# Optimization experiments

Hardware: AMD Instinct MI355X
Metric: run time of the kernel (lower is better)

The kernel has to match this reference:

```python
import jax, jax.numpy as jnp
import numpy as np

K = 5            # neighborhood kernel size
PAD = 2
CENTER = (K * K) // 2   # index 12: the pixel itself
TEMP = 0.1       # InfoNCE temperature
EPS = 1e-8
NUM_CLASSES = 2


def _patches_f(x):
    """x: [B,H,W,C] float -> [B,H,W,K*K,C] zero-padded 5x5 neighborhoods."""
    B, H, W, C = x.shape
    xp = jnp.pad(x, ((0, 0), (PAD, PAD), (PAD, PAD), (0, 0)))
    return jnp.stack([xp[:, i:i + H, j:j + W, :]
                      for i in range(K) for j in range(K)], axis=3)


def _patches_i(x):
    """x: [B,H,W] int -> [B,H,W,K*K] zero-padded 5x5 neighborhoods."""
    B, H, W = x.shape
    xp = jnp.pad(x, ((0, 0), (PAD, PAD), (PAD, PAD)))
    return jnp.stack([xp[:, i:i + H, j:j + W]
                      for i in range(K) for j in range(K)], axis=3)


def setup_inputs() -> dict:
    key = jax.random.key(0)
    k1, k2, k3, k4 = jax.random.split(key, 4)
    B, C, H, W = 2, 256, 96, 96
    return {
        "er_input": jax.random.normal(k1, (B, C, H, W), dtype=jnp.float32),
        "seg_logit": jax.random.normal(k2, (B, NUM_CLASSES, H, W), dtype=jnp.float32),
        "seg_label": jax.random.randint(k3, (B, H, W), 0, NUM_CLASSES, dtype=jnp.int32),
        "gt_boundary_seg": jax.random.randint(k4, (B, H, W), 0, 2, dtype=jnp.int32),
    }


def reference(er_input, seg_logit, seg_label, gt_boundary_seg):
    # er_input: [B,C,H,W]; seg_logit: [B,nc,H,W]; labels: [B,H,W]
    feat = er_input.transpose(0, 2, 3, 1)          # [B,H,W,C]
    pred = jnp.argmax(seg_logit, axis=1)           # [B,H,W]
    gt_b = jnp.where(gt_boundary_seg == 255, 0, gt_boundary_seg)
    edge = gt_b.astype(bool)                       # boundary mask [B,H,W]

    neigh_feat = _patches_f(feat)                  # [B,H,W,25,C]
    neigh_label = _patches_i(seg_label)            # [B,H,W,25]
    neigh_pred = _patches_i(pred)                  # [B,H,W,25]

    def correct(c):
        # one_hot(label)*one_hot(pred) at class c, per neighbor
        return ((neigh_label == c) & (neigh_pred == c)).astype(feat.dtype)

    a_norm_neigh = jnp.linalg.norm(neigh_feat, axis=-1)   # [B,H,W,25]

    total = jnp.asarray(0.0, dtype=feat.dtype)
    shown = list(range(NUM_CLASSES))               # shown_class (both assumed present)
    n_cls = len(shown)
    for i in range(n_cls):
        c = shown[i]
        c_pre = shown[(i - 1) % n_cls]
        c_post = shown[(i + 1) % n_cls]

        now_mask = (seg_label == c)                # [B,H,W]
        neigh_is_c = (neigh_label == c).astype(feat.dtype)
        # same-class neighbor count, center excluded (kernel has 0 at center)
        count = neigh_is_c.sum(-1) - neigh_is_c[..., CENTER]
        pix_mask = ((count >= 1) & edge & now_mask).astype(feat.dtype)  # [B,H,W]

        w_now = correct(c)                         # [B,H,W,25]
        w_neg = correct(c_pre) + correct(c_post)   # pre_class + post_class weights

        # anchor = center feature * correct indicator (taken before zeroing center)
        anchor = neigh_feat[..., CENTER, :] * w_now[..., CENTER, None]  # [B,H,W,C]
        # positive = mean over 25 neighbors of (feat * correct), center zeroed
        positive = (jnp.einsum('bhwkc,bhwk->bhwc', neigh_feat, w_now) - anchor) / (K * K)

        a_norm = jnp.linalg.norm(anchor, axis=-1)  # [B,H,W]
        p_norm = jnp.linalg.norm(positive, axis=-1)
        pos_cos = (anchor * positive).sum(-1) / (a_norm * p_norm + EPS)   # [B,H,W]

        # negatives: per-offset features weighted by (pre+post) correctness
        dots = jnp.einsum('bhwc,bhwkc->bhwk', anchor, neigh_feat)         # [B,H,W,25]
        neg_cos = (dots * w_neg) / (a_norm[..., None] * a_norm_neigh * w_neg + EPS)

        logits = jnp.concatenate([pos_cos[..., None], neg_cos], axis=-1) / TEMP
        loss_pix = -jax.nn.log_softmax(logits, axis=-1)[..., 0]          # [B,H,W]

        total = total + (loss_pix * pix_mask).sum() / jnp.maximum(pix_mask.sum(), 1.0)
    return total
```

## Files before the change

### kernel.cpp

```cpp
#include <hip/hip_runtime.h>
#include <math.h>

#define Hc 96
#define Wc 96
#define Bc 2
#define Cc 256
#define HWc (Hc * Wc)
#define NKc 25
#define NPIX (Bc * HWc)
#define NSLOT 32

#define OFF_ACC 0
#define OFF_CNT 256
#define OFF_MIS 264
#define OFF_HC 272
#define OFF_DONE 276
#define HDR_FLOATS 80
#define OFF_NRM2 320
#define OFF_META (OFF_NRM2 + 2 * NPIX * 4)
#define OFF_WL (OFF_META + NPIX)
#define OFF_FT (OFF_WL + NPIX * 16)

__device__ __forceinline__ float wave_reduce_sum(float v) {
#pragma unroll
  for (int off = 32; off > 0; off >>= 1) v += __shfl_xor(v, off);
  return v;
}

#define NOFF(k) (((k) / 5 - 2) * Wc + ((k) % 5 - 2))

__device__ __forceinline__ unsigned f2bf_pack(float lo, float hi) {
  unsigned a = __float_as_uint(lo), b = __float_as_uint(hi);
  a = (a + 0x7FFFu + ((a >> 16) & 1u)) >> 16;
  b = (b + 0x7FFFu + ((b >> 16) & 1u)) >> 16;
  return a | (b << 16);
}
__device__ __forceinline__ float bf2f(unsigned short u) {
  return __uint_as_float(((unsigned)u) << 16);
}

__global__ __launch_bounds__(256) void transpose_kernel(
    const float* __restrict__ in, const float* __restrict__ seg_logit,
    const int* __restrict__ seg_label, unsigned* __restrict__ outb,
    float* __restrict__ nrm2h, unsigned char* __restrict__ meta,
    float* __restrict__ hdr) {
  __shared__ float tile[64][33];
  __shared__ float part[8][32];
  const int bx = blockIdx.x;
  const int b = blockIdx.y;
  const int half = blockIdx.z;
  const int tx = threadIdx.x;
  const int ty = threadIdx.y;
  const float* src = in + (size_t)b * Cc * HWc;
  const int p0 = bx * 32;

  if (bx == 0 && b == 0 && half == 0) {
    const int t = ty * 32 + tx;
    if (t < HDR_FLOATS) hdr[t] = 0.f;
  }

  float psum = 0.f;
  for (int s = 0; s < 2; ++s) {
    const int c0 = half * 128 + s * 64;
#pragma unroll
    for (int i = 0; i < 8; i++)
      tile[ty + i * 8][tx] = src[(size_t)(c0 + ty + i * 8) * HWc + p0 + tx];
    __syncthreads();
#pragma unroll
    for (int i = 0; i < 4; i++) {
      const int px = ty + i * 8;
      const unsigned pk = f2bf_pack(tile[2 * tx][px], tile[2 * tx + 1][px]);
      outb[(size_t)(b * HWc + p0 + px) * (Cc / 2) + (c0 / 2) + tx] = pk;
    }
#pragma unroll
    for (int j = 0; j < 8; j++) {
      const float v = tile[ty * 8 + j][tx];
      psum += v * v;
    }
    __syncthreads();
  }
  part[ty][tx] = psum;
  __syncthreads();
  if (ty == 0) {
    float t = 0.f;
#pragma unroll
    for (int j = 0; j < 8; j++) t += part[j][tx];
    const int hw = p0 + tx;
    const int gi = b * HWc + hw;
    nrm2h[half * NPIX + gi] = t;
    if (half == 0) {
      const float l0 = seg_logit[(size_t)(b * 2 + 0) * HWc + hw];
      const float l1 = seg_logit[(size_t)(b * 2 + 1) * HWc + hw];
      const int pr = (l1 > l0) ? 1 : 0;
      meta[gi] = (unsigned char)((seg_label[gi] & 1) | (pr << 1));
    }
  }
}

__global__ __launch_bounds__(256) void classify_kernel(
    const unsigned char* __restrict__ meta, const int* __restrict__ gtb,
    const float* __restrict__ nrm2h, float* __restrict__ cnt,
    float* __restrict__ mis, unsigned int* __restrict__ heavyCount,
    uint4* __restrict__ worklist) {
  __shared__ unsigned int s_cnt[4];
  if (threadIdx.x < 4) s_cnt[threadIdx.x] = 0;
  __syncthreads();
  const int tid = blockIdx.x * 256 + threadIdx.x;
  bool heavy = false;
  int c = 0;
  unsigned mNow = 0, mNeg = 0;
  float a_norm = 0.f;
  {
    const int hw = tid % HWc;
    const int h = hw / Wc, w = hw % Wc;
    int g = gtb[tid];
    if (g == 255) g = 0;
    if (g) {
      const int m0 = meta[tid];
      c = m0 & 1;
      const int pc = (m0 >> 1) & 1;
      const int oc = 1 - c;
      int count = 0;
#pragma unroll
      for (int k = 0; k < NKc; k++) {
        const int di = k / 5 - 2, dj = k % 5 - 2;
        const int hh = h + di, ww = w + dj;
        const bool inb = (hh >= 0) && (hh < Hc) && (ww >= 0) && (ww < Wc);
        const int mv = inb ? (int)meta[tid + di * Wc + dj] : 0;
        const int lb = mv & 1, pr = (mv >> 1) & 1;
        count += (lb == c);
        if (inb) {
          if (lb == c && pr == c) mNow |= 1u << k;
          if (lb == oc && pr == oc) mNeg |= 1u << k;
        }
      }
      count -= 1;
      if (count >= 1) {
        atomicAdd(&s_cnt[c], 1u);
        if (pc == c) {
          heavy = true;
          a_norm = sqrtf(nrm2h[tid] + nrm2h[NPIX + tid]);
        } else {
          atomicAdd(&s_cnt[2 + c], 1u);
        }
      }
    }
  }
  const unsigned long long m = __ballot(heavy);
  const int lane = threadIdx.x & 63;
  if (m) {
    unsigned int base = 0;
    if (lane == 0) base = atomicAdd(heavyCount, (unsigned)__popcll(m));
    base = __shfl(base, 0);
    if (heavy) {
      const unsigned idx = base + (unsigned)__popcll(m & ((1ull << lane) - 1ull));
      worklist[idx] = make_uint4((unsigned)tid | ((unsigned)c << 16), mNow, mNeg,
                                 __float_as_uint(a_norm));
    }
  }
  __syncthreads();
  if (threadIdx.x < 2) {
    if (s_cnt[threadIdx.x]) atomicAdd(&cnt[threadIdx.x], (float)s_cnt[threadIdx.x]);
    if (s_cnt[2 + threadIdx.x]) atomicAdd(&mis[threadIdx.x], (float)s_cnt[2 + threadIdx.x]);
  }
}

__global__ __launch_bounds__(256, 2) void heavy_kernel(
    const ushort4* __restrict__ ftb, const float* __restrict__ nrm2h,
    const unsigned int* __restrict__ heavyCount,
    const uint4* __restrict__ worklist, float* __restrict__ accum,
    unsigned int* __restrict__ doneCnt, const float* __restrict__ cnt,
    const float* __restrict__ mis, float* __restrict__ out) {
  __shared__ float s_loss[2];
  __shared__ unsigned s_last;
  if (threadIdx.x < 2) s_loss[threadIdx.x] = 0.f;
  __syncthreads();
  const int lane = threadIdx.x & 63;
  const int wv = threadIdx.x >> 6;
  const unsigned nH = *heavyCount;
  const unsigned nw = gridDim.x * 4;
  float lacc0 = 0.f, lacc1 = 0.f;
  for (unsigned i = blockIdx.x * 4 + wv; i < nH; i += nw) {
    const uint4 e = worklist[i];
    const int wid = e.x & 0xffff;
    const int c = (e.x >> 16) & 1;
    const unsigned mNow = e.y, mNeg = e.z;
    const unsigned mAny = mNow | mNeg;
    const float a_norm = __uint_as_float(e.w);

    const int dlt = (lane / 5 - 2) * Wc + (lane % 5 - 2);
    const int nbn = (lane < NKc && ((mNeg >> lane) & 1u)) ? wid + dlt : wid;
    const float nk2a = nrm2h[nbn];
    const float nk2b = nrm2h[NPIX + nbn];
    const ushort4 a4 = ftb[(size_t)wid * 64 + lane];
    ushort4 f4[NKc];
#pragma unroll
    for (int k = 0; k < NKc; k++) {
      const int off = ((mAny >> k) & 1u) ? wid + NOFF(k) : wid;
      f4[k] = ftb[(size_t)off * 64 + lane];
    }
    asm volatile("" ::: "memory");

    const float ax = bf2f(a4.x), ay = bf2f(a4.y), az = bf2f(a4.z), aw = bf2f(a4.w);
    const float nkv = sqrtf(nk2a + nk2b);

    float4 pos = make_float4(0.f, 0.f, 0.f, 0.f);
#pragma unroll
    for (int k = 0; k < NKc; k++) {
      const float wN = (float)((mNow >> k) & 1u);
      pos.x = fmaf(bf2f(f4[k].x), wN, pos.x);
      pos.y = fmaf(bf2f(f4[k].y), wN, pos.y);
      pos.z = fmaf(bf2f(f4[k].z), wN, pos.z);
      pos.w = fmaf(bf2f(f4[k].w), wN, pos.w);
    }
    float4 pv;
    pv.x = (pos.x - ax) * (1.0f / 25.0f);
    pv.y = (pos.y - ay) * (1.0f / 25.0f);
    pv.z = (pos.z - az) * (1.0f / 25.0f);
    pv.w = (pos.w - aw) * (1.0f / 25.0f);
    const float p2 = wave_reduce_sum(pv.x * pv.x + pv.y * pv.y + pv.z * pv.z + pv.w * pv.w);
    const float ad = wave_reduce_sum(ax * pv.x + ay * pv.y + az * pv.z + aw * pv.w);
    const float x0 = (ad / (a_norm * sqrtf(p2) + 1e-8f)) * 10.0f;

    float mx = fmaxf(x0, 0.f);
    float ssum = __expf(x0 - mx) + (float)(NKc - __popc(mNeg)) * __expf(-mx);
#pragma unroll
    for (int k = 0; k < NKc; k++) {
      if ((mNeg >> k) & 1u) {
        const float d = wave_reduce_sum(ax * bf2f(f4[k].x) + ay * bf2f(f4[k].y) +
                                        az * bf2f(f4[k].z) + aw * bf2f(f4[k].w));
        const float nk = __shfl(nkv, k);
        const float x = ((d * 2.0f) / (a_norm * nk * 2.0f + 1e-8f)) * 10.0f;
        if (x > mx) {
          ssum = ssum * __expf(mx - x) + 1.0f;
          mx = x;
        } else {
          ssum += __expf(x - mx);
        }
      }
    }
    const float loss = mx + __logf(ssum) - x0;
    if (lane == 0) {
      if (c == 0) lacc0 += loss; else lacc1 += loss;
    }
  }
  if (lane == 0) {
    if (lacc0 != 0.f) atomicAdd(&s_loss[0], lacc0);
    if (lacc1 != 0.f) atomicAdd(&s_loss[1], lacc1);
  }
  __syncthreads();
  if (threadIdx.x < 2) {
    const float v = s_loss[threadIdx.x];
    if (v != 0.f) atomicAdd(&accum[(blockIdx.x & (NSLOT - 1)) * 2 + threadIdx.x], v);
  }
  __syncthreads();
  if (threadIdx.x == 0)
    s_last = (atomicAdd(doneCnt, 1u) == (unsigned)(gridDim.x - 1)) ? 1u : 0u;
  __syncthreads();
  if (s_last && threadIdx.x < NSLOT * 2) {
    const float v = atomicAdd(&accum[threadIdx.x], 0.0f);
    float v0 = (threadIdx.x & 1) ? 0.f : v;
    float v1 = (threadIdx.x & 1) ? v : 0.f;
    v0 = wave_reduce_sum(v0);
    v1 = wave_reduce_sum(v1);
    if (threadIdx.x == 0) {
      const float LOG26 = logf(26.0f);
      out[0] = (v0 + LOG26 * mis[0]) / fmaxf(cnt[0], 1.0f) +
               (v1 + LOG26 * mis[1]) / fmaxf(cnt[1], 1.0f);
    }
  }
}

extern "C" void kernel_launch(void* const* d_in, const int* in_sizes, int n_in,
                              void* d_out, int out_size, void* d_ws, size_t ws_size,
                              hipStream_t stream) {
  const float* er = (const float*)d_in[0];
  const float* seg_logit = (const float*)d_in[1];
  const int* seg_label = (const int*)d_in[2];
  const int* gtb = (const int*)d_in[3];
  float* out = (float*)d_out;

  char* ws = (char*)d_ws;
  float* hdr = (float*)ws;
  float* accum = (float*)(ws + OFF_ACC);
  float* cnt = (float*)(ws + OFF_CNT);
  float* mis = (float*)(ws + OFF_MIS);
  unsigned int* heavyCount = (unsigned int*)(ws + OFF_HC);
  unsigned int* doneCnt = (unsigned int*)(ws + OFF_DONE);
  float* nrm2h = (float*)(ws + OFF_NRM2);
  unsigned char* meta = (unsigned char*)(ws + OFF_META);
  uint4* worklist = (uint4*)(ws + OFF_WL);
  unsigned* featTb = (unsigned*)(ws + OFF_FT);

  dim3 tb(32, 8, 1);
  dim3 tg(HWc / 32, Bc, 2);
  transpose_kernel<<<tg, tb, 0, stream>>>(er, seg_logit, seg_label, featTb,
                                          nrm2h, meta, hdr);

  classify_kernel<<<NPIX / 256, 256, 0, stream>>>(meta, gtb, nrm2h, cnt, mis,
                                                  heavyCount, worklist);

  heavy_kernel<<<1152, 256, 0, stream>>>((const ushort4*)featTb, nrm2h,
                                         heavyCount, worklist, accum, doneCnt,
                                         cnt, mis, out);
}
```

Measured before the change: 45.53 us.

## Fuse pixel classification into transpose kernel and use dense per-pixel worklist

```diff
diff --git a/kernel.cpp b/kernel.cpp
--- a/kernel.cpp
+++ b/kernel.cpp
@@ -9,17 +9,14 @@
 #define NKc 25
 #define NPIX (Bc * HWc)
 #define NSLOT 32
+#define NBLK 576
 
 #define OFF_ACC 0
-#define OFF_CNT 256
-#define OFF_MIS 264
-#define OFF_HC 272
-#define OFF_DONE 276
-#define HDR_FLOATS 80
-#define OFF_NRM2 320
-#define OFF_META (OFF_NRM2 + 2 * NPIX * 4)
-#define OFF_WL (OFF_META + NPIX)
-#define OFF_FT (OFF_WL + NPIX * 16)
+#define OFF_DONE 256
+#define OFF_CNTB 512
+#define OFF_NRM2 4096
+#define OFF_WL 151552
+#define OFF_FT 446464
 
 __device__ __forceinline__ float wave_reduce_sum(float v) {
 #pragma unroll
@@ -39,25 +36,25 @@
   return __uint_as_float(((unsigned)u) << 16);
 }
 
-__global__ __launch_bounds__(256) void transpose_kernel(
+__global__ __launch_bounds__(256) void transclass_kernel(
     const float* __restrict__ in, const float* __restrict__ seg_logit,
-    const int* __restrict__ seg_label, unsigned* __restrict__ outb,
-    float* __restrict__ nrm2h, unsigned char* __restrict__ meta,
+    const int* __restrict__ seg_label, const int* __restrict__ gtb,
+    unsigned* __restrict__ outb, float* __restrict__ nrm2h,
+    uint4* __restrict__ wl, unsigned* __restrict__ cntBlk,
     float* __restrict__ hdr) {
   __shared__ float tile[64][33];
   __shared__ float part[8][32];
+  __shared__ unsigned s_ccnt[4];
   const int bx = blockIdx.x;
   const int b = blockIdx.y;
   const int half = blockIdx.z;
   const int tx = threadIdx.x;
   const int ty = threadIdx.y;
+  const int flat = ty * 32 + tx;
   const float* src = in + (size_t)b * Cc * HWc;
   const int p0 = bx * 32;
 
-  if (bx == 0 && b == 0 && half == 0) {
-    const int t = ty * 32 + tx;
-    if (t < HDR_FLOATS) hdr[t] = 0.f;
-  }
+  if (bx == 0 && b == 0 && half == 0 && flat < 80) hdr[flat] = 0.f;
 
   float psum = 0.f;
   for (int s = 0; s < 2; ++s) {
@@ -85,109 +82,77 @@
     float t = 0.f;
 #pragma unroll
     for (int j = 0; j < 8; j++) t += part[j][tx];
-    const int hw = p0 + tx;
-    const int gi = b * HWc + hw;
-    nrm2h[half * NPIX + gi] = t;
-    if (half == 0) {
-      const float l0 = seg_logit[(size_t)(b * 2 + 0) * HWc + hw];
-      const float l1 = seg_logit[(size_t)(b * 2 + 1) * HWc + hw];
-      const int pr = (l1 > l0) ? 1 : 0;
-      meta[gi] = (unsigned char)((seg_label[gi] & 1) | (pr << 1));
-    }
-  }
-}
-
-__global__ __launch_bounds__(256) void classify_kernel(
-    const unsigned char* __restrict__ meta, const int* __restrict__ gtb,
-    const float* __restrict__ nrm2h, float* __restrict__ cnt,
-    float* __restrict__ mis, unsigned int* __restrict__ heavyCount,
-    uint4* __restrict__ worklist) {
-  __shared__ unsigned int s_cnt[4];
-  if (threadIdx.x < 4) s_cnt[threadIdx.x] = 0;
-  __syncthreads();
-  const int tid = blockIdx.x * 256 + threadIdx.x;
-  bool heavy = false;
-  int c = 0;
-  unsigned mNow = 0, mNeg = 0;
-  float a_norm = 0.f;
-  {
-    const int hw = tid % HWc;
-    const int h = hw / Wc, w = hw % Wc;
-    int g = gtb[tid];
-    if (g == 255) g = 0;
-    if (g) {
-      const int m0 = meta[tid];
-      c = m0 & 1;
-      const int pc = (m0 >> 1) & 1;
-      const int oc = 1 - c;
-      int count = 0;
-#pragma unroll
-      for (int k = 0; k < NKc; k++) {
-        const int di = k / 5 - 2, dj = k % 5 - 2;
+    nrm2h[half * NPIX + b * HWc + p0 + tx] = t;
+  }
+
+  if (half == 0) {
+    const int lane = flat & 63;
+    const int wv = flat >> 6;
+    unsigned wsum = 0;
+    for (int px = 0; px < 8; ++px) {
+      const int hw = p0 + wv * 8 + px;
+      const int tid = b * HWc + hw;
+      const int h = hw / Wc, w = hw - h * Wc;
+      int g = gtb[tid];
+      if (g == 255) g = 0;
+      int lb = 0, pr = 0;
+      bool inb = false;
+      if (lane < NKc) {
+        const int di = lane / 5 - 2, dj = lane % 5 - 2;
         const int hh = h + di, ww = w + dj;
-        const bool inb = (hh >= 0) && (hh < Hc) && (ww >= 0) && (ww < Wc);
-        const int mv = inb ? (int)meta[tid + di * Wc + dj] : 0;
-        const int lb = mv & 1, pr = (mv >> 1) & 1;
-        count += (lb == c);
+        inb = (hh >= 0) && (hh < Hc) && (ww >= 0) && (ww < Wc);
         if (inb) {
-          if (lb == c && pr == c) mNow |= 1u << k;
-          if (lb == oc && pr == oc) mNeg |= 1u << k;
+          const int d = di * Wc + dj;
+          lb = seg_label[tid + d];
+          const float l0 = seg_logit[(size_t)(b * 2 + 0) * HWc + hw + d];
+          const float l1 = seg_logit[(size_t)(b * 2 + 1) * HWc + hw + d];
+          pr = (l1 > l0) ? 1 : 0;
         }
       }
-      count -= 1;
-      if (count >= 1) {
-        atomicAdd(&s_cnt[c], 1u);
-        if (pc == c) {
-          heavy = true;
-          a_norm = sqrtf(nrm2h[tid] + nrm2h[NPIX + tid]);
-        } else {
-          atomicAdd(&s_cnt[2 + c], 1u);
-        }
-      }
-    }
-  }
-  const unsigned long long m = __ballot(heavy);
-  const int lane = threadIdx.x & 63;
-  if (m) {
-    unsigned int base = 0;
-    if (lane == 0) base = atomicAdd(heavyCount, (unsigned)__popcll(m));
-    base = __shfl(base, 0);
-    if (heavy) {
-      const unsigned idx = base + (unsigned)__popcll(m & ((1ull << lane) - 1ull));
-      worklist[idx] = make_uint4((unsigned)tid | ((unsigned)c << 16), mNow, mNeg,
-                                 __float_as_uint(a_norm));
-    }
-  }
-  __syncthreads();
-  if (threadIdx.x < 2) {
-    if (s_cnt[threadIdx.x]) atomicAdd(&cnt[threadIdx.x], (float)s_cnt[threadIdx.x]);
-    if (s_cnt[2 + threadIdx.x]) atomicAdd(&mis[threadIdx.x], (float)s_cnt[2 + threadIdx.x]);
+      const int c = __shfl(lb, 12);
+      const int pc = __shfl(pr, 12);
+      const int count =
+          __popcll(__ballot(lane < NKc && lb == c)) - 1;
+      const bool valid = (g != 0) && (count >= 1);
+      const unsigned mNow =
+          (unsigned)__ballot(lane < NKc && inb && lb == c && pr == c);
+      const unsigned mNeg =
+          (unsigned)__ballot(lane < NKc && inb && lb == (1 - c) && pr == (1 - c));
+      const bool hv = valid && (pc == c);
+      if (lane == 0)
+        wl[tid] = make_uint4(hv ? (1u | ((unsigned)c << 1)) : 0u, mNow, mNeg, 0u);
+      wsum += valid ? ((1u << (8 * c)) + ((pc != c) ? (1u << (16 + 8 * c)) : 0u))
+                    : 0u;
+    }
+    if (lane == 0) s_ccnt[wv] = wsum;
+    __syncthreads();
+    if (flat == 0)
+      cntBlk[b * 288 + bx] = s_ccnt[0] + s_ccnt[1] + s_ccnt[2] + s_ccnt[3];
   }
 }
 
 __global__ __launch_bounds__(256, 2) void heavy_kernel(
     const ushort4* __restrict__ ftb, const float* __restrict__ nrm2h,
-    const unsigned int* __restrict__ heavyCount,
-    const uint4* __restrict__ worklist, float* __restrict__ accum,
-    unsigned int* __restrict__ doneCnt, const float* __restrict__ cnt,
-    const float* __restrict__ mis, float* __restrict__ out) {
+    const uint4* __restrict__ wl, float* __restrict__ accum,
+    unsigned int* __restrict__ doneCnt, const unsigned* __restrict__ cntBlk,
+    float* __restrict__ out) {
   __shared__ float s_loss[2];
   __shared__ unsigned s_last;
   if (threadIdx.x < 2) s_loss[threadIdx.x] = 0.f;
   __syncthreads();
   const int lane = threadIdx.x & 63;
   const int wv = threadIdx.x >> 6;
-  const unsigned nH = *heavyCount;
   const unsigned nw = gridDim.x * 4;
   float lacc0 = 0.f, lacc1 = 0.f;
-  for (unsigned i = blockIdx.x * 4 + wv; i < nH; i += nw) {
-    const uint4 e = worklist[i];
-    const int wid = e.x & 0xffff;
-    const int c = (e.x >> 16) & 1;
+  for (unsigned i = blockIdx.x * 4 + wv; i < NPIX; i += nw) {
+    const uint4 e = wl[i];
+    if (!(e.x & 1u)) continue;
+    const int wid = (int)i;
+    const int c = (e.x >> 1) & 1;
     const unsigned mNow = e.y, mNeg = e.z;
     const unsigned mAny = mNow | mNeg;
-    const float a_norm = __uint_as_float(e.w);
-
+
+    const float a_norm = sqrtf(nrm2h[wid] + nrm2h[NPIX + wid]);
     const int dlt = (lane / 5 - 2) * Wc + (lane % 5 - 2);
     const int nbn = (lane < NKc && ((mNeg >> lane) & 1u)) ? wid + dlt : wid;
     const float nk2a = nrm2h[nbn];
@@ -257,16 +222,30 @@
   if (threadIdx.x == 0)
     s_last = (atomicAdd(doneCnt, 1u) == (unsigned)(gridDim.x - 1)) ? 1u : 0u;
   __syncthreads();
-  if (s_last && threadIdx.x < NSLOT * 2) {
-    const float v = atomicAdd(&accum[threadIdx.x], 0.0f);
-    float v0 = (threadIdx.x & 1) ? 0.f : v;
-    float v1 = (threadIdx.x & 1) ? v : 0.f;
-    v0 = wave_reduce_sum(v0);
-    v1 = wave_reduce_sum(v1);
-    if (threadIdx.x == 0) {
+  if (s_last && threadIdx.x < 64) {
+    const int t = threadIdx.x;
+    const float v = atomicAdd(&accum[t], 0.0f);
+    float l0 = (t & 1) ? 0.f : v;
+    float l1 = (t & 1) ? v : 0.f;
+    unsigned pc0 = 0, pc1 = 0, pm0 = 0, pm1 = 0;
+#pragma unroll
+    for (int j = 0; j < 9; j++) {
+      const unsigned u = cntBlk[t * 9 + j];
+      pc0 += u & 0xFFu;
+      pc1 += (u >> 8) & 0xFFu;
+      pm0 += (u >> 16) & 0xFFu;
+      pm1 += (u >> 24) & 0xFFu;
+    }
+    l0 = wave_reduce_sum(l0);
+    l1 = wave_reduce_sum(l1);
+    const float c0 = wave_reduce_sum((float)pc0);
+    const float c1 = wave_reduce_sum((float)pc1);
+    const float m0 = wave_reduce_sum((float)pm0);
+    const float m1 = wave_reduce_sum((float)pm1);
+    if (t == 0) {
       const float LOG26 = logf(26.0f);
-      out[0] = (v0 + LOG26 * mis[0]) / fmaxf(cnt[0], 1.0f) +
-               (v1 + LOG26 * mis[1]) / fmaxf(cnt[1], 1.0f);
+      out[0] = (l0 + LOG26 * m0) / fmaxf(c0, 1.0f) +
+               (l1 + LOG26 * m1) / fmaxf(c1, 1.0f);
     }
   }
 }
@@ -283,24 +262,17 @@
   char* ws = (char*)d_ws;
   float* hdr = (float*)ws;
   float* accum = (float*)(ws + OFF_ACC);
-  float* cnt = (float*)(ws + OFF_CNT);
-  float* mis = (float*)(ws + OFF_MIS);
-  unsigned int* heavyCount = (unsigned int*)(ws + OFF_HC);
   unsigned int* doneCnt = (unsigned int*)(ws + OFF_DONE);
+  unsigned* cntBlk = (unsigned*)(ws + OFF_CNTB);
   float* nrm2h = (float*)(ws + OFF_NRM2);
-  unsigned char* meta = (unsigned char*)(ws + OFF_META);
-  uint4* worklist = (uint4*)(ws + OFF_WL);
+  uint4* wl = (uint4*)(ws + OFF_WL);
   unsigned* featTb = (unsigned*)(ws + OFF_FT);
 
   dim3 tb(32, 8, 1);
   dim3 tg(HWc / 32, Bc, 2);
-  transpose_kernel<<<tg, tb, 0, stream>>>(er, seg_logit, seg_label, featTb,
-                                          nrm2h, meta, hdr);
-
-  classify_kernel<<<NPIX / 256, 256, 0, stream>>>(meta, gtb, nrm2h, cnt, mis,
-                                                  heavyCount, worklist);
-
-  heavy_kernel<<<1152, 256, 0, stream>>>((const ushort4*)featTb, nrm2h,
-                                         heavyCount, worklist, accum, doneCnt,
-                                         cnt, mis, out);
-}
+  transclass_kernel<<<tg, tb, 0, stream>>>(er, seg_logit, seg_label, gtb,
+                                           featTb, nrm2h, wl, cntBlk, hdr);
+
+  heavy_kernel<<<1152, 256, 0, stream>>>((const ushort4*)featTb, nrm2h, wl,
+                                         accum, doneCnt, cntBlk, out);
+}
```

Result: faster. 43.35 us (median of 2 runs) (-4.8%).
